# Performance work log

Hardware: AMD Instinct MI355X
Metric: run time of the kernel (lower is better)

Reference implementation:

```python
import jax, jax.numpy as jnp
import numpy as np

ALPHA = 0.7
N = 4194304
NUM_ACTIONS = 3


def setup_inputs() -> dict:
    key = jax.random.key(0)
    k1, k2, k3, k4, k5 = jax.random.split(key, 5)
    return {
        "pred_prices": jax.random.normal(k1, (N,), dtype=jnp.float32),
        "pred_actions": jax.random.normal(k2, (N, NUM_ACTIONS), dtype=jnp.float32),
        "tgt_prices": jax.random.normal(k3, (N,), dtype=jnp.float32),
        "tgt_actions": jax.random.randint(k4, (N,), 0, NUM_ACTIONS, dtype=jnp.int64),
        "prices": jax.random.normal(k5, (N,), dtype=jnp.float32),
    }


def reference(pred_prices, pred_actions, tgt_prices, tgt_actions, prices):
    # MSE over price predictions
    price_loss = jnp.mean((pred_prices - tgt_prices) ** 2)

    # Cross-entropy (mean over batch), matches nn.CrossEntropyLoss on logits
    logp = jax.nn.log_softmax(pred_actions, axis=-1)  # [N, 3]
    action_loss = -jnp.mean(jnp.take_along_axis(logp, tgt_actions[:, None], axis=-1))

    # Vectorized replacement of the per-sample profit loop (no_grad in original)
    predicted_actions = jnp.argmax(pred_actions, axis=-1)  # [N]
    p = tgt_prices
    d = p[1:] - p[:-1]                     # [N-1]
    zero = jnp.zeros((1,), p.dtype)
    diff_fwd = jnp.concatenate([d, zero])  # p[i+1]-p[i], last entry 0
    diff_bwd = jnp.concatenate([zero, d])  # p[i]-p[i-1], first entry 0
    profits = jnp.where(predicted_actions == 0, diff_fwd,
                        jnp.where(predicted_actions == 2, diff_bwd,
                                  jnp.zeros_like(p)))
    profit_weight = jax.nn.sigmoid(profits * 10.0)
    weighted_action_loss = action_loss * jnp.mean(profit_weight)

    return ALPHA * weighted_action_loss + (1.0 - ALPHA) * price_loss
```

## Files before the change

### kernel.cpp

```cpp
#include <hip/hip_runtime.h>

static constexpr int NN = 4194304;

__global__ __launch_bounds__(256) void pfl_main(
    const float* __restrict__ pp,
    const float* __restrict__ pa,
    const float* __restrict__ tp,
    const int*   __restrict__ ta,
    double* __restrict__ acc)
{
    const int G = NN / 4;
    float sq = 0.f, ce = 0.f, pw = 0.f;

    const float4* pp4 = (const float4*)pp;
    const float4* tp4 = (const float4*)tp;
    const float4* pa4 = (const float4*)pa;
    const int4*   ta4 = (const int4*)ta;

    for (int g = blockIdx.x * blockDim.x + threadIdx.x; g < G;
         g += gridDim.x * blockDim.x) {
        const int i = g * 4;
        float4 p  = pp4[g];
        float4 t  = tp4[g];
        int4   a  = ta4[g];
        float4 A0 = pa4[3*g + 0];
        float4 A1 = pa4[3*g + 1];
        float4 A2 = pa4[3*g + 2];

        float tm1  = (i > 0)      ? tp[i - 1] : 0.f;
        float tnx  = (i + 4 < NN) ? tp[i + 4] : 0.f;

        float tv[6]     = {tm1, t.x, t.y, t.z, t.w, tnx};
        float pv[4]     = {p.x, p.y, p.z, p.w};
        float rows[4][3] = {{A0.x, A0.y, A0.z},
                            {A0.w, A1.x, A1.y},
                            {A1.z, A1.w, A2.x},
                            {A2.y, A2.z, A2.w}};
        int av[4] = {a.x, a.y, a.z, a.w};

        #pragma unroll
        for (int j = 0; j < 4; ++j) {
            const int idx = i + j;
            float d = pv[j] - tv[j + 1];
            sq += d * d;

            float x0 = rows[j][0], x1 = rows[j][1], x2 = rows[j][2];
            float m  = fmaxf(x0, fmaxf(x1, x2));
            float lse = m + __logf(__expf(x0 - m) + __expf(x1 - m) + __expf(x2 - m));
            float tgt = (av[j] == 0) ? x0 : ((av[j] == 1) ? x1 : x2);
            ce += lse - tgt;

            int   pidx = 0;
            float best = x0;
            if (x1 > best) { best = x1; pidx = 1; }
            if (x2 > best) { pidx = 2; }

            float profit = 0.f;
            if (pidx == 0)      profit = (idx + 1 < NN) ? (tv[j + 2] - tv[j + 1]) : 0.f;
            else if (pidx == 2) profit = (idx > 0)      ? (tv[j + 1] - tv[j])     : 0.f;

            pw += 1.f / (1.f + __expf(-10.f * profit));
        }
    }

    #pragma unroll
    for (int off = 32; off > 0; off >>= 1) {
        sq += __shfl_down(sq, off, 64);
        ce += __shfl_down(ce, off, 64);
        pw += __shfl_down(pw, off, 64);
    }

    __shared__ float s_sq[4], s_ce[4], s_pw[4];
    const int lane = threadIdx.x & 63;
    const int wid  = threadIdx.x >> 6;
    if (lane == 0) { s_sq[wid] = sq; s_ce[wid] = ce; s_pw[wid] = pw; }
    __syncthreads();

    if (threadIdx.x == 0) {
        float tsq = s_sq[0] + s_sq[1] + s_sq[2] + s_sq[3];
        float tce = s_ce[0] + s_ce[1] + s_ce[2] + s_ce[3];
        float tpw = s_pw[0] + s_pw[1] + s_pw[2] + s_pw[3];
        atomicAdd(&acc[0], (double)tsq);
        atomicAdd(&acc[1], (double)tce);
        atomicAdd(&acc[2], (double)tpw);
    }
}

__global__ void pfl_final(const double* __restrict__ acc, float* __restrict__ out) {
    const double inv = 1.0 / (double)NN;
    double price_loss  = acc[0] * inv;
    double action_loss = acc[1] * inv;
    double mean_pw     = acc[2] * inv;
    out[0] = (float)(0.7 * action_loss * mean_pw + 0.3 * price_loss);
}

extern "C" void kernel_launch(void* const* d_in, const int* in_sizes, int n_in,
                              void* d_out, int out_size, void* d_ws, size_t ws_size,
                              hipStream_t stream) {
    const float* pp = (const float*)d_in[0];
    const float* pa = (const float*)d_in[1];
    const float* tp = (const float*)d_in[2];
    const int*   ta = (const int*)d_in[3];

    double* acc = (double*)d_ws;
    hipMemsetAsync(acc, 0, 3 * sizeof(double), stream);

    pfl_main<<<1024, 256, 0, stream>>>(pp, pa, tp, ta, acc);
    pfl_final<<<1, 1, 0, stream>>>(acc, (float*)d_out);
}
```

Baseline: 164.6 us.

## Replace atomics with per-block partials and batch loads per thread

The grid-stride loop is replaced by a fixed grid of 2048 blocks, each thread handling exactly two float4 groups whose loads are all issued before any compute, which raises memory-level parallelism. The double-precision atomics and the memset are dropped in favour of per-block float partial sums written to the workspace and reduced by a 256-thread final kernel. This removes one launch and atomic contention, at the cost of hardcoding the grid to the problem size and holding more registers per thread.

```diff
diff --git a/kernel.cpp b/kernel.cpp
--- a/kernel.cpp
+++ b/kernel.cpp
@@ -1,42 +1,57 @@
 #include <hip/hip_runtime.h>
 
-static constexpr int NN = 4194304;
+static constexpr int NN  = 4194304;
+static constexpr int NB  = 2048;
+static constexpr int TPB = 256;
+static constexpr int GPT = 2;
 
 __global__ __launch_bounds__(256) void pfl_main(
     const float* __restrict__ pp,
     const float* __restrict__ pa,
     const float* __restrict__ tp,
     const int*   __restrict__ ta,
-    double* __restrict__ acc)
+    float* __restrict__ bsum)
 {
-    const int G = NN / 4;
-    float sq = 0.f, ce = 0.f, pw = 0.f;
+    const int tid  = threadIdx.x;
+    const int bid  = blockIdx.x;
+    const int base = bid * (TPB * GPT);
 
     const float4* pp4 = (const float4*)pp;
     const float4* tp4 = (const float4*)tp;
     const float4* pa4 = (const float4*)pa;
     const int4*   ta4 = (const int4*)ta;
 
-    for (int g = blockIdx.x * blockDim.x + threadIdx.x; g < G;
-         g += gridDim.x * blockDim.x) {
+    float4 p[GPT], t[GPT], A0[GPT], A1[GPT], A2[GPT];
+    int4   a[GPT];
+    float  tm1[GPT], tnx[GPT];
+
+    #pragma unroll
+    for (int k = 0; k < GPT; ++k) {
+        const int g = base + k * TPB + tid;
         const int i = g * 4;
-        float4 p  = pp4[g];
-        float4 t  = tp4[g];
-        int4   a  = ta4[g];
-        float4 A0 = pa4[3*g + 0];
-        float4 A1 = pa4[3*g + 1];
-        float4 A2 = pa4[3*g + 2];
+        p[k]  = pp4[g];
+        t[k]  = tp4[g];
+        a[k]  = ta4[g];
+        A0[k] = pa4[3*g + 0];
+        A1[k] = pa4[3*g + 1];
+        A2[k] = pa4[3*g + 2];
+        tm1[k] = (i > 0)      ? tp[i - 1] : 0.f;
+        tnx[k] = (i + 4 < NN) ? tp[i + 4] : 0.f;
+    }
 
-        float tm1  = (i > 0)      ? tp[i - 1] : 0.f;
-        float tnx  = (i + 4 < NN) ? tp[i + 4] : 0.f;
+    float sq = 0.f, ce = 0.f, pw = 0.f;
 
-        float tv[6]     = {tm1, t.x, t.y, t.z, t.w, tnx};
-        float pv[4]     = {p.x, p.y, p.z, p.w};
-        float rows[4][3] = {{A0.x, A0.y, A0.z},
-                            {A0.w, A1.x, A1.y},
-                            {A1.z, A1.w, A2.x},
-                            {A2.y, A2.z, A2.w}};
-        int av[4] = {a.x, a.y, a.z, a.w};
+    #pragma unroll
+    for (int k = 0; k < GPT; ++k) {
+        const int g = base + k * TPB + tid;
+        const int i = g * 4;
+        float tv[6] = {tm1[k], t[k].x, t[k].y, t[k].z, t[k].w, tnx[k]};
+        float pv[4] = {p[k].x, p[k].y, p[k].z, p[k].w};
+        float rows[4][3] = {{A0[k].x, A0[k].y, A0[k].z},
+                            {A0[k].w, A1[k].x, A1[k].y},
+                            {A1[k].z, A1[k].w, A2[k].x},
+                            {A2[k].y, A2[k].z, A2[k].w}};
+        int av[4] = {a[k].x, a[k].y, a[k].z, a[k].w};
 
         #pragma unroll
         for (int j = 0; j < 4; ++j) {
@@ -50,7 +65,7 @@
             float tgt = (av[j] == 0) ? x0 : ((av[j] == 1) ? x1 : x2);
             ce += lse - tgt;
 
-            int   pidx = 0;
+            int pidx = 0;
             float best = x0;
             if (x1 > best) { best = x1; pidx = 1; }
             if (x2 > best) { pidx = 2; }
@@ -71,27 +86,45 @@
     }
 
     __shared__ float s_sq[4], s_ce[4], s_pw[4];
+    const int lane = tid & 63;
+    const int wid  = tid >> 6;
+    if (lane == 0) { s_sq[wid] = sq; s_ce[wid] = ce; s_pw[wid] = pw; }
+    __syncthreads();
+
+    if (tid == 0) {
+        bsum[bid]          = s_sq[0] + s_sq[1] + s_sq[2] + s_sq[3];
+        bsum[NB + bid]     = s_ce[0] + s_ce[1] + s_ce[2] + s_ce[3];
+        bsum[2 * NB + bid] = s_pw[0] + s_pw[1] + s_pw[2] + s_pw[3];
+    }
+}
+
+__global__ __launch_bounds__(256) void pfl_final(const float* __restrict__ bsum,
+                                                 float* __restrict__ out) {
+    double sq = 0.0, ce = 0.0, pw = 0.0;
+    for (int i = threadIdx.x; i < NB; i += 256) {
+        sq += (double)bsum[i];
+        ce += (double)bsum[NB + i];
+        pw += (double)bsum[2 * NB + i];
+    }
+    #pragma unroll
+    for (int off = 32; off > 0; off >>= 1) {
+        sq += __shfl_down(sq, off, 64);
+        ce += __shfl_down(ce, off, 64);
+        pw += __shfl_down(pw, off, 64);
+    }
+    __shared__ double s_sq[4], s_ce[4], s_pw[4];
     const int lane = threadIdx.x & 63;
     const int wid  = threadIdx.x >> 6;
     if (lane == 0) { s_sq[wid] = sq; s_ce[wid] = ce; s_pw[wid] = pw; }
     __syncthreads();
 
     if (threadIdx.x == 0) {
-        float tsq = s_sq[0] + s_sq[1] + s_sq[2] + s_sq[3];
-        float tce = s_ce[0] + s_ce[1] + s_ce[2] + s_ce[3];
-        float tpw = s_pw[0] + s_pw[1] + s_pw[2] + s_pw[3];
-        atomicAdd(&acc[0], (double)tsq);
-        atomicAdd(&acc[1], (double)tce);
-        atomicAdd(&acc[2], (double)tpw);
+        double tsq = s_sq[0] + s_sq[1] + s_sq[2] + s_sq[3];
+        double tce = s_ce[0] + s_ce[1] + s_ce[2] + s_ce[3];
+        double tpw = s_pw[0] + s_pw[1] + s_pw[2] + s_pw[3];
+        const double inv = 1.0 / (double)NN;
+        out[0] = (float)(0.7 * (tce * inv) * (tpw * inv) + 0.3 * (tsq * inv));
     }
-}
-
-__global__ void pfl_final(const double* __restrict__ acc, float* __restrict__ out) {
-    const double inv = 1.0 / (double)NN;
-    double price_loss  = acc[0] * inv;
-    double action_loss = acc[1] * inv;
-    double mean_pw     = acc[2] * inv;
-    out[0] = (float)(0.7 * action_loss * mean_pw + 0.3 * price_loss);
 }
 
 extern "C" void kernel_launch(void* const* d_in, const int* in_sizes, int n_in,
@@ -102,9 +135,8 @@
     const float* tp = (const float*)d_in[2];
     const int*   ta = (const int*)d_in[3];
 
-    double* acc = (double*)d_ws;
-    hipMemsetAsync(acc, 0, 3 * sizeof(double), stream);
+    float* bsum = (float*)d_ws;
 
-    pfl_main<<<1024, 256, 0, stream>>>(pp, pa, tp, ta, acc);
-    pfl_final<<<1, 1, 0, stream>>>(acc, (float*)d_out);
+    pfl_main<<<NB, TPB, 0, stream>>>(pp, pa, tp, ta, bsum);
+    pfl_final<<<1, TPB, 0, stream>>>(bsum, (float*)d_out);
 }
```

Result: faster. 136.2 us (-17.3%).
